# Performance work log

Hardware: AMD Instinct MI355X
Metric: run time of the kernel (lower is better)

The kernel has to match this reference:

```python
import jax, jax.numpy as jnp
import numpy as np

WS = 11
SIGMA = 1.5
L = 1.0  # val_range


def _gaussian_window(ws=WS, sigma=SIGMA):
    x = np.arange(ws, dtype=np.float64) - ws // 2
    g = np.exp(-(x ** 2) / (2.0 * sigma ** 2))
    g = g / g.sum()
    w2d = np.outer(g, g)
    return jnp.asarray(w2d, dtype=jnp.float32)  # [ws, ws]


def _depthwise_blur(x, w2d):
    # x: [B, C, H, W]; depthwise gaussian conv with SAME-style padding ws//2
    c = x.shape[1]
    kern = jnp.broadcast_to(w2d, (c, 1, WS, WS)).astype(x.dtype)  # OIHW, groups=C
    pad = WS // 2
    return jax.lax.conv_general_dilated(
        x, kern, window_strides=(1, 1), padding=[(pad, pad), (pad, pad)],
        dimension_numbers=('NCHW', 'OIHW', 'NCHW'), feature_group_count=c)


def setup_inputs() -> dict:
    key = jax.random.key(0)
    k1, k2 = jax.random.split(key)
    img1 = jax.random.uniform(k1, (32, 3, 512, 512), dtype=jnp.float32)
    img2 = jax.random.uniform(k2, (32, 3, 512, 512), dtype=jnp.float32)
    return {"img1": img1, "img2": img2}


def reference(img1, img2):
    w2d = _gaussian_window()
    mu1 = _depthwise_blur(img1, w2d)
    mu2 = _depthwise_blur(img2, w2d)
    mu1_sq = mu1 * mu1
    mu2_sq = mu2 * mu2
    mu1_mu2 = mu1 * mu2
    sigma1_sq = _depthwise_blur(img1 * img1, w2d) - mu1_sq
    sigma2_sq = _depthwise_blur(img2 * img2, w2d) - mu2_sq
    sigma12 = _depthwise_blur(img1 * img2, w2d) - mu1_mu2
    C1 = (0.01 * L) ** 2
    C2 = (0.03 * L) ** 2
    ssim_map = ((2.0 * mu1_mu2 + C1) * (2.0 * sigma12 + C2)) / (
        (mu1_sq + mu2_sq + C1) * (sigma1_sq + sigma2_sq + C2))
    return 1.0 - ssim_map.mean()
```

## Files before the change

### kernel.cpp

```cpp
#include <hip/hip_runtime.h>
#include <math.h>

typedef _Float16 f16;
typedef _Float16 f16x8 __attribute__((ext_vector_type(8)));
typedef _Float16 f16x4 __attribute__((ext_vector_type(4)));
typedef float f32x4 __attribute__((ext_vector_type(4)));

#define ROWS 88
#define NTHREADS 256

__device__ __forceinline__ float ssim_px(float m1, float m2, float mss, float m12) {
  const float C1 = 0.0001f, C2 = 0.0009f;
  const float mu1s = m1 * m1, mu2s = m2 * m2, mu12 = m1 * m2;
  const float num = (2.f * mu12 + C1) * (2.f * (m12 - mu12) + C2);
  const float den = (mu1s + mu2s + C1) * (mss - mu1s - mu2s + C2);
  return num * __builtin_amdgcn_rcpf(den);
}

template <bool MASKED>
__device__ __forceinline__ void issue_loads(
    const float* __restrict__ p1, const float* __restrict__ p2,
    int gy0, int xb, int n,
    float4 La0[5], float4 La1[5], float4 Lb0[5], float4 Lb1[5], float okf[5])
{
#pragma unroll
  for (int rg = 0; rg < 5; rg++) {
    const int rimg = gy0 + rg * 16 + n;
    size_t base;
    if (MASKED) {
      const bool octok = (xb >= 0) && (xb <= 504);
      const bool rok = (rimg >= 0) && (rimg < 512);
      okf[rg] = (rok && octok) ? 1.f : 0.f;
      const int rc = rok ? rimg : 0;
      const int xc = octok ? xb : 0;
      base = ((size_t)rc << 9) + (size_t)xc;
    } else {
      okf[rg] = 1.f;
      base = ((size_t)rimg << 9) + (size_t)xb;
    }
    La0[rg] = *(const float4*)(p1 + base);
    La1[rg] = *(const float4*)(p1 + base + 4);
    Lb0[rg] = *(const float4*)(p2 + base);
    Lb1[rg] = *(const float4*)(p2 + base + 4);
  }
}

template <bool MASKED>
__device__ __forceinline__ void h_consume(
    const float4 La0[5], const float4 La1[5],
    const float4 Lb0[5], const float4 Lb1[5], const float okf[5],
    f16 (*si)[64][ROWS], int px, int kg, const f16x8& Bh)
{
#pragma unroll
  for (int rg = 0; rg < 5; rg++) {
    const float av[8] = {La0[rg].x, La0[rg].y, La0[rg].z, La0[rg].w,
                         La1[rg].x, La1[rg].y, La1[rg].z, La1[rg].w};
    const float bw[8] = {Lb0[rg].x, Lb0[rg].y, Lb0[rg].z, Lb0[rg].w,
                         Lb1[rg].x, Lb1[rg].y, Lb1[rg].z, Lb1[rg].w};
    f16x8 fa, fb;
#pragma unroll
    for (int i = 0; i < 8; i++) {
      float ai = av[i], bi = bw[i];
      if (MASKED) { ai *= okf[rg]; bi *= okf[rg]; }
      fa[i] = (f16)ai;
      fb[i] = (f16)bi;
    }
    const f16x8 fp = fa * fb;
    const f16x8 fs = fa * fa + fb * fb;
    const f32x4 z = {0.f, 0.f, 0.f, 0.f};
    const f32x4 Da = __builtin_amdgcn_mfma_f32_16x16x32_f16(fa, Bh, z, 0, 0, 0);
    const f32x4 Db = __builtin_amdgcn_mfma_f32_16x16x32_f16(fb, Bh, z, 0, 0, 0);
    const f32x4 Ds = __builtin_amdgcn_mfma_f32_16x16x32_f16(fs, Bh, z, 0, 0, 0);
    const f32x4 Dp = __builtin_amdgcn_mfma_f32_16x16x32_f16(fp, Bh, z, 0, 0, 0);
    const int sr = rg * 16 + kg * 4;
    const f16x4 wa = {(f16)Da[0], (f16)Da[1], (f16)Da[2], (f16)Da[3]};
    const f16x4 wb = {(f16)Db[0], (f16)Db[1], (f16)Db[2], (f16)Db[3]};
    const f16x4 ws = {(f16)Ds[0], (f16)Ds[1], (f16)Ds[2], (f16)Ds[3]};
    const f16x4 wp = {(f16)Dp[0], (f16)Dp[1], (f16)Dp[2], (f16)Dp[3]};
    *(f16x4*)&si[0][px][sr] = wa;
    *(f16x4*)&si[1][px][sr] = wb;
    *(f16x4*)&si[2][px][sr] = ws;
    *(f16x4*)&si[3][px][sr] = wp;
  }
}

__device__ __forceinline__ void v_phase(
    f16 (*si)[64][ROWS], int px, int kg, const f16x8& Av, float acc4[4])
{
#pragma unroll
  for (int og = 0; og < 4; og++) {
    const int srb = og * 16 + 8 * kg;
    const f16x8 Ba = *(const f16x8*)&si[0][px][srb];
    const f16x8 Bb = *(const f16x8*)&si[1][px][srb];
    const f16x8 Bs = *(const f16x8*)&si[2][px][srb];
    const f16x8 Bp = *(const f16x8*)&si[3][px][srb];
    const f32x4 z = {0.f, 0.f, 0.f, 0.f};
    const f32x4 Ma = __builtin_amdgcn_mfma_f32_16x16x32_f16(Av, Ba, z, 0, 0, 0);
    const f32x4 Mb = __builtin_amdgcn_mfma_f32_16x16x32_f16(Av, Bb, z, 0, 0, 0);
    const f32x4 Ms = __builtin_amdgcn_mfma_f32_16x16x32_f16(Av, Bs, z, 0, 0, 0);
    const f32x4 Mp = __builtin_amdgcn_mfma_f32_16x16x32_f16(Av, Bp, z, 0, 0, 0);
#pragma unroll
    for (int r = 0; r < 4; r++)
      acc4[r] += ssim_px(Ma[r], Mb[r], Ms[r], Mp[r]);
  }
}

__global__ __launch_bounds__(NTHREADS) void ssim_main_kernel(
    const float* __restrict__ img1, const float* __restrict__ img2,
    float* __restrict__ partials, float norm, float cexp)
{
  __shared__ f16 si[4][64][ROWS];
  __shared__ float sred[4];

  const int tid = threadIdx.x;
  const int wv = tid >> 6, lane = tid & 63;
  const int n = lane & 15, kg = lane >> 4;

  int b = blockIdx.x;
  const int tx = b & 7; b >>= 3;
  const int ty = b & 7; b >>= 3;
  const float* __restrict__ p1A = img1 + (size_t)b * 262144;
  const float* __restrict__ p2A = img2 + (size_t)b * 262144;
  const float* __restrict__ p1B = p1A + (size_t)48 * 262144;
  const float* __restrict__ p2B = p2A + (size_t)48 * 262144;

  f16x8 Bh, Av;
#pragma unroll
  for (int i = 0; i < 8; i++) {
    const int k = 8 * kg + i;
    {
      const int idx = k - n - 3;
      const float d = (float)(idx - 5);
      const float val = norm * exp2f(cexp * d * d);
      Bh[i] = (idx >= 0 && idx <= 10) ? (f16)val : (f16)0.f;
    }
    {
      const int idx = k - n;
      const float d = (float)(idx - 5);
      const float val = norm * exp2f(cexp * d * d);
      Av[i] = (idx >= 0 && idx <= 10) ? (f16)val : (f16)0.f;
    }
  }

  const int X0 = tx * 64 + wv * 16;
  const int xb = X0 - 8 + 8 * kg;
  const int gy0 = ty * 64 - 5;
  const int px = wv * 16 + n;
  const bool interior = (tx >= 1) && (tx <= 6) && (ty >= 1) && (ty <= 6);

  float acc4[4] = {0.f, 0.f, 0.f, 0.f};
  float4 La0[5], La1[5], Lb0[5], Lb1[5];
  float okf[5];

  if (interior) {
    issue_loads<false>(p1A, p2A, gy0, xb, n, La0, La1, Lb0, Lb1, okf);
    h_consume<false>(La0, La1, Lb0, Lb1, okf, si, px, kg, Bh);
  } else {
    issue_loads<true>(p1A, p2A, gy0, xb, n, La0, La1, Lb0, Lb1, okf);
    h_consume<true>(La0, La1, Lb0, Lb1, okf, si, px, kg, Bh);
  }

  __builtin_amdgcn_sched_barrier(0);
  if (interior)
    issue_loads<false>(p1B, p2B, gy0, xb, n, La0, La1, Lb0, Lb1, okf);
  else
    issue_loads<true>(p1B, p2B, gy0, xb, n, La0, La1, Lb0, Lb1, okf);
  __builtin_amdgcn_sched_barrier(0);

  __syncthreads();

  v_phase(si, px, kg, Av, acc4);
  __syncthreads();

  if (interior)
    h_consume<false>(La0, La1, Lb0, Lb1, okf, si, px, kg, Bh);
  else
    h_consume<true>(La0, La1, Lb0, Lb1, okf, si, px, kg, Bh);
  __syncthreads();

  v_phase(si, px, kg, Av, acc4);

  float accSum = (acc4[0] + acc4[1]) + (acc4[2] + acc4[3]);

  for (int off = 32; off > 0; off >>= 1)
    accSum += __shfl_down(accSum, off, 64);
  if (lane == 0) sred[wv] = accSum;
  __syncthreads();
  if (tid == 0)
    partials[blockIdx.x] = sred[0] + sred[1] + sred[2] + sred[3];
}

__global__ __launch_bounds__(256) void ssim_final_kernel(
    const float* __restrict__ partials, float* __restrict__ out,
    int n, double invN)
{
  __shared__ double sred[4];
  const int tid = threadIdx.x;
  double s = 0.0;
  for (int i = tid; i < n; i += 256) s += (double)partials[i];
  for (int off = 32; off > 0; off >>= 1)
    s += __shfl_down(s, off, 64);
  if ((tid & 63) == 0) sred[tid >> 6] = s;
  __syncthreads();
  if (tid == 0) {
    double tot = 0.0;
#pragma unroll
    for (int i = 0; i < 4; i++) tot += sred[i];
    out[0] = (float)(1.0 - tot * invN);
  }
}

extern "C" void kernel_launch(void* const* d_in, const int* in_sizes, int n_in,
                              void* d_out, int out_size, void* d_ws, size_t ws_size,
                              hipStream_t stream) {
  const float* img1 = (const float*)d_in[0];
  const float* img2 = (const float*)d_in[1];
  float* out = (float*)d_out;
  float* partials = (float*)d_ws;

  const int planes = in_sizes[0] / (512 * 512);
  const int nBlocks = (planes / 2) * 8 * 8;

  double sum = 0.0;
  for (int i = 0; i < 11; i++) {
    const double x = (double)(i - 5);
    sum += exp(-(x * x) / 4.5);
  }
  const float norm = (float)(1.0 / sum);
  const float cexp = (float)(-1.0 / (4.5 * 0.6931471805599453));

  const double invN = 1.0 / (double)in_sizes[0];

  ssim_main_kernel<<<nBlocks, NTHREADS, 0, stream>>>(img1, img2, partials, norm, cexp);
  ssim_final_kernel<<<1, 256, 0, stream>>>(partials, out, nBlocks, invN);
}
```

Baseline: 80.95 us.

## Make each block sweep a full column strip of one plane with software-pipelined loads

Each block now owns a 64-wide column strip of one plane and walks all 8 row tiles in a loop, prefetching the next tile's loads while doing the vertical pass on the current one. Before, each block handled one 64x64 tile for two planes. The grid shrinks from 3072 to 768 blocks (8 per plane) and the per-block work grows. This is meant to amortise the filter-weight setup and keep loads overlapped with compute over more iterations. In exchange it leaves fewer blocks to fill the GPU, adds a serial dependency chain per block, and the hardcoded 96 planes assumes the test shape.

```diff
diff --git a/kernel.cpp b/kernel.cpp
--- a/kernel.cpp
+++ b/kernel.cpp
@@ -116,13 +116,11 @@
   const int wv = tid >> 6, lane = tid & 63;
   const int n = lane & 15, kg = lane >> 4;
 
-  int b = blockIdx.x;
-  const int tx = b & 7; b >>= 3;
-  const int ty = b & 7; b >>= 3;
-  const float* __restrict__ p1A = img1 + (size_t)b * 262144;
-  const float* __restrict__ p2A = img2 + (size_t)b * 262144;
-  const float* __restrict__ p1B = p1A + (size_t)48 * 262144;
-  const float* __restrict__ p2B = p2A + (size_t)48 * 262144;
+  const int b = blockIdx.x;
+  const int tx = b / 96;
+  const int plane = b - tx * 96;
+  const float* __restrict__ p1 = img1 + (size_t)plane * 262144;
+  const float* __restrict__ p2 = img2 + (size_t)plane * 262144;
 
   f16x8 Bh, Av;
 #pragma unroll
@@ -144,41 +142,37 @@
 
   const int X0 = tx * 64 + wv * 16;
   const int xb = X0 - 8 + 8 * kg;
-  const int gy0 = ty * 64 - 5;
   const int px = wv * 16 + n;
-  const bool interior = (tx >= 1) && (tx <= 6) && (ty >= 1) && (ty <= 6);
+  const bool edgeX = (tx == 0) || (tx == 7);
 
   float acc4[4] = {0.f, 0.f, 0.f, 0.f};
   float4 La0[5], La1[5], Lb0[5], Lb1[5];
   float okf[5];
 
-  if (interior) {
-    issue_loads<false>(p1A, p2A, gy0, xb, n, La0, La1, Lb0, Lb1, okf);
-    h_consume<false>(La0, La1, Lb0, Lb1, okf, si, px, kg, Bh);
-  } else {
-    issue_loads<true>(p1A, p2A, gy0, xb, n, La0, La1, Lb0, Lb1, okf);
-    h_consume<true>(La0, La1, Lb0, Lb1, okf, si, px, kg, Bh);
-  }
-
-  __builtin_amdgcn_sched_barrier(0);
-  if (interior)
-    issue_loads<false>(p1B, p2B, gy0, xb, n, La0, La1, Lb0, Lb1, okf);
-  else
-    issue_loads<true>(p1B, p2B, gy0, xb, n, La0, La1, Lb0, Lb1, okf);
-  __builtin_amdgcn_sched_barrier(0);
-
-  __syncthreads();
-
-  v_phase(si, px, kg, Av, acc4);
-  __syncthreads();
-
-  if (interior)
-    h_consume<false>(La0, La1, Lb0, Lb1, okf, si, px, kg, Bh);
-  else
-    h_consume<true>(La0, La1, Lb0, Lb1, okf, si, px, kg, Bh);
-  __syncthreads();
-
-  v_phase(si, px, kg, Av, acc4);
+  issue_loads<true>(p1, p2, -5, xb, n, La0, La1, Lb0, Lb1, okf);
+  h_consume<true>(La0, La1, Lb0, Lb1, okf, si, px, kg, Bh);
+
+#pragma unroll 1
+  for (int t = 0; t < 8; ++t) {
+    if (t < 7) {
+      const int gy0n = (t + 1) * 64 - 5;
+      __builtin_amdgcn_sched_barrier(0);
+      if (edgeX || t == 6)
+        issue_loads<true>(p1, p2, gy0n, xb, n, La0, La1, Lb0, Lb1, okf);
+      else
+        issue_loads<false>(p1, p2, gy0n, xb, n, La0, La1, Lb0, Lb1, okf);
+      __builtin_amdgcn_sched_barrier(0);
+    }
+    __syncthreads();
+    v_phase(si, px, kg, Av, acc4);
+    __syncthreads();
+    if (t < 7) {
+      if (edgeX || t == 6)
+        h_consume<true>(La0, La1, Lb0, Lb1, okf, si, px, kg, Bh);
+      else
+        h_consume<false>(La0, La1, Lb0, Lb1, okf, si, px, kg, Bh);
+    }
+  }
 
   float accSum = (acc4[0] + acc4[1]) + (acc4[2] + acc4[3]);
 
@@ -219,7 +213,7 @@
   float* partials = (float*)d_ws;
 
   const int planes = in_sizes[0] / (512 * 512);
-  const int nBlocks = (planes / 2) * 8 * 8;
+  const int nBlocks = 8 * planes;
 
   double sum = 0.0;
   for (int i = 0; i < 11; i++) {
```

Result: slower. 90.85 us (+12.2%).
